# Kernel tuning notes

Hardware: AMD Instinct MI355X
Metric: run time of the kernel (lower is better)

## Reference

```python
import jax, jax.numpy as jnp
import numpy as np

B, S, D, A = 64, 2048, 512, 512


def setup_inputs() -> dict:
    key = jax.random.key(0)
    ks = jax.random.split(key, 6)
    return {
        "input": jax.random.normal(ks[0], (B, D), dtype=jnp.float32),
        "context": jax.random.normal(ks[1], (B, S, D), dtype=jnp.float32),
        "Wh": jax.random.uniform(ks[2], (D, A), dtype=jnp.float32, minval=-0.1, maxval=0.1),
        "Ws": jax.random.uniform(ks[3], (D, A), dtype=jnp.float32, minval=-0.1, maxval=0.1),
        "b_attn": jax.random.uniform(ks[4], (A,), dtype=jnp.float32, minval=-0.1, maxval=0.1),
        "va": jax.random.uniform(ks[5], (A,), dtype=jnp.float32, minval=-0.1, maxval=0.1),
    }


def reference(input, context, Wh, Ws, b_attn, va):
    # _concat score: tanh(ht@Wh + context@Ws + b) @ va  -> [B, S]
    ht_proj = input @ Wh                      # [B, A]
    ctx_proj = jnp.einsum("bsd,da->bsa", context, Ws)  # [B, S, A]
    concat = jnp.tanh(ht_proj[:, None, :] + ctx_proj + b_attn)  # [B, S, A]
    attn = jnp.einsum("bsa,a->bs", concat, va)  # [B, S]
    # padding mask: positions whose mean feature is exactly 0
    context_mask = jnp.mean(context, axis=-1) == 0  # [B, S]
    attn = jnp.where(context_mask, -jnp.inf, attn)
    attn_dist = jax.nn.softmax(attn, axis=1)  # [B, S]
    attn_context = jnp.einsum("bsd,bs->bd", context, attn_dist)  # [B, D]
    return attn_context, attn_dist
```

## Files before the change

kernel.cpp:

```cpp
#include <hip/hip_runtime.h>
#include <hip/hip_bf16.h>
#include <math.h>

#define B_ 64
#define S_ 2048
#define D_ 512
#define A_ 512

typedef __attribute__((ext_vector_type(8))) short short8;
typedef __attribute__((ext_vector_type(4))) short short4b;
typedef __attribute__((ext_vector_type(4))) float f32x4;

__device__ __forceinline__ short bf16b(float f) {
    __hip_bfloat16 h = __float2bfloat16(f);
    union { __hip_bfloat16 h; short s; } u; u.h = h;
    return u.s;
}

__device__ __forceinline__ float tanh_fast(float x) {
    float e = __expf(2.0f * x);
    return 1.0f - 2.0f / (e + 1.0f);
}

__device__ __forceinline__ void llds16(const void* g, void* l) {
    __builtin_amdgcn_global_load_lds(
        (const __attribute__((address_space(1))) unsigned int*)g,
        (__attribute__((address_space(3))) unsigned int*)l, 16, 0, 0);
}

__global__ __launch_bounds__(256) void k_htw(const float* __restrict__ input,
                                             const float* __restrict__ Wh,
                                             const float* __restrict__ b_attn,
                                             float* __restrict__ htWb) {
    __shared__ float xin[512];
    const int b = blockIdx.x, t = threadIdx.x;
    xin[t] = input[b * D_ + t];
    xin[t + 256] = input[b * D_ + t + 256];
    __syncthreads();
    float a0 = 0.f, a1 = 0.f;
#pragma unroll 8
    for (int d = 0; d < D_; ++d) {
        const float xv = xin[d];
        a0 += xv * Wh[d * A_ + t];
        a1 += xv * Wh[d * A_ + t + 256];
    }
    htWb[b * A_ + t] = a0 + b_attn[t];
    htWb[b * A_ + t + 256] = a1 + b_attn[t + 256];
}

__global__ __launch_bounds__(256) void k_wst(const float* __restrict__ Ws,
                                             short* __restrict__ WsT) {
    const int bx = blockIdx.x & 7, by = blockIdx.x >> 3;
    const int r0 = by * 64, c0 = bx * 64;
    __shared__ short tile[64][72];
    const int t = threadIdx.x;
    const int row = t >> 4, col4 = (t & 15) * 4;
#pragma unroll
    for (int i = 0; i < 4; ++i) {
        const float4 v = *(const float4*)&Ws[(r0 + row + i * 16) * A_ + c0 + col4];
        tile[col4 + 0][row + i * 16] = bf16b(v.x);
        tile[col4 + 1][row + i * 16] = bf16b(v.y);
        tile[col4 + 2][row + i * 16] = bf16b(v.z);
        tile[col4 + 3][row + i * 16] = bf16b(v.w);
    }
    __syncthreads();
#pragma unroll
    for (int i = 0; i < 4; ++i) {
        const int arow = row + i * 16;
        short4b o;
        o.x = tile[arow][col4 + 0];
        o.y = tile[arow][col4 + 1];
        o.z = tile[arow][col4 + 2];
        o.w = tile[arow][col4 + 3];
        *(short4b*)&WsT[(c0 + arow) * D_ + r0 + col4] = o;
    }
}

__global__ __launch_bounds__(512, 2)
void k_score2(const float* __restrict__ ctx, const short* __restrict__ WsT,
              const float* __restrict__ htWb, const float* __restrict__ va,
              float* __restrict__ scores) {
    __shared__ __align__(16) short Ab[2][128 * 32];
    __shared__ __align__(16) short Bb[2][512 * 32];
    __shared__ float hv_s[512];
    __shared__ float va_s[512];
    __shared__ float scores_s[128];
    __shared__ float rowsum_s[128];

    const int tid = threadIdx.x;
    const int w = tid >> 6, lane = tid & 63;
    const int wm = w >> 2, wn = w & 3;
    const int blk = blockIdx.x;
    const int b = blk >> 4;
    const int s0 = (blk & 15) * 128;
    const long rowbase = (long)b * S_ + s0;

    hv_s[tid] = htWb[b * A_ + tid];
    va_s[tid] = va[tid];
    if (tid < 128) scores_s[tid] = 0.f;

    const int arow = tid >> 2, aq = tid & 2 * 2 - 1;
    const float* aSrc = ctx + (rowbase + arow) * (long)D_;
    float rowsum_acc = 0.f;

    f32x4 acc[4][8];
#pragma unroll
    for (int i = 0; i < 4; ++i)
#pragma unroll
        for (int j = 0; j < 8; ++j)
#pragma unroll
            for (int e = 0; e < 4; ++e) acc[i][j][e] = 0.f;

#define STAGE_B(buf, kt)                                                      \
    {                                                                         \
        _Pragma("unroll") for (int j = 0; j < 4; ++j) {                       \
            const int a = (w * 4 + j) * 16 + (lane >> 2);                     \
            const int c = lane & 3;                                           \
            const int csw = c ^ ((a >> 1) & 3);                               \
            llds16(WsT + a * D_ + (kt) * 32 + csw * 8,                        \
                   (void*)&Bb[buf][(w * 4 + j) * 512]);                       \
        }                                                                     \
    }

#define STAGE_A_WRITE(buf, v0, v1)                                            \
    {                                                                         \
        rowsum_acc += (v0).x + (v0).y + (v0).z + (v0).w;                      \
        rowsum_acc += (v1).x + (v1).y + (v1).z + (v1).w;                      \
        short4b o0, o1;                                                       \
        o0.x = bf16b((v0).x); o0.y = bf16b((v0).y);                           \
        o0.z = bf16b((v0).z); o0.w = bf16b((v0).w);                           \
        o1.x = bf16b((v1).x); o1.y = bf16b((v1).y);                           \
        o1.z = bf16b((v1).z); o1.w = bf16b((v1).w);                           \
        const int sw = (arow >> 1) & 3;                                       \
        const int c0 = (aq >> 1), c1 = 2 + (aq >> 1), sub = aq & 1;           \
        *(short4b*)((char*)&Ab[buf][0] + arow * 64 + ((c0 ^ sw) * 16) + sub * 8) = o0; \
        *(short4b*)((char*)&Ab[buf][0] + arow * 64 + ((c1 ^ sw) * 16) + sub * 8) = o1; \
    }

    STAGE_B(0, 0);
    {
        const float4 v0 = *(const float4*)(aSrc + aq * 4);
        const float4 v1 = *(const float4*)(aSrc + aq * 4 + 16);
        STAGE_A_WRITE(0, v0, v1);
    }
    __syncthreads();

    for (int kt = 0; kt < 16; ++kt) {
        const int cur = kt & 1;
        float4 nv0, nv1;
        if (kt < 15) {
            STAGE_B(cur ^ 1, kt + 1);
            nv0 = *(const float4*)(aSrc + (kt + 1) * 32 + aq * 4);
            nv1 = *(const float4*)(aSrc + (kt + 1) * 32 + aq * 4 + 16);
        }
        {
            short8 af[4];
#pragma unroll
            for (int mf = 0; mf < 4; ++mf) {
                const int r = wm * 64 + mf * 16 + (lane & 15);
                const int c = lane >> 4;
                const int csw = c ^ ((r >> 1) & 3);
                af[mf] = *(const short8*)((const char*)&Ab[cur][0] + r * 64 + csw * 16);
            }
#pragma unroll
            for (int nf = 0; nf < 8; ++nf) {
                const int a = wn * 128 + nf * 16 + (lane & 15);
                const int c = lane >> 4;
                const int csw = c ^ ((a >> 1) & 3);
                const short8 bf =
                    *(const short8*)((const char*)&Bb[cur][0] + a * 64 + csw * 16);
#pragma unroll
                for (int mf = 0; mf < 4; ++mf)
                    acc[mf][nf] = __builtin_amdgcn_mfma_f32_16x16x32_bf16(
                        af[mf], bf, acc[mf][nf], 0, 0, 0);
            }
        }
        if (kt < 15) STAGE_A_WRITE(cur ^ 1, nv0, nv1);
        __syncthreads();
    }

    rowsum_acc += __shfl_xor(rowsum_acc, 1);
    rowsum_acc += __shfl_xor(rowsum_acc, 2);
    if ((tid & 3) == 0) rowsum_s[arow] = rowsum_acc;

    float hv[8], vv[8];
#pragma unroll
    for (int nf = 0; nf < 8; ++nf) {
        const int col = wn * 128 + nf * 16 + (lane & 15);
        hv[nf] = hv_s[col];
        vv[nf] = va_s[col];
    }
#pragma unroll
    for (int mf = 0; mf < 4; ++mf) {
#pragma unroll
        for (int e = 0; e < 4; ++e) {
            float p = 0.f;
#pragma unroll
            for (int nf = 0; nf < 8; ++nf)
                p += vv[nf] * tanh_fast(hv[nf] + acc[mf][nf][e]);
            p += __shfl_xor(p, 1);
            p += __shfl_xor(p, 2);
            p += __shfl_xor(p, 4);
            p += __shfl_xor(p, 8);
            if ((lane & 15) == 0) {
                const int row = wm * 64 + mf * 16 + (lane >> 4) * 4 + e;
                atomicAdd(&scores_s[row], p);
            }
        }
    }
    __syncthreads();

    if (tid < 128) {
        float sc = scores_s[tid];
        if (rowsum_s[tid] == 0.0f) sc = -__builtin_inff();
        scores[rowbase + tid] = sc;
    }
}

__global__ __launch_bounds__(256) void k_softmax(float* __restrict__ dist) {
    const int b = blockIdx.x, t = threadIdx.x;
    float* p = dist + b * S_;
    float v[8];
    float m = -__builtin_inff();
#pragma unroll
    for (int i = 0; i < 8; ++i) {
        v[i] = p[t + i * 256];
        m = fmaxf(m, v[i]);
    }
#pragma unroll
    for (int mask = 1; mask < 64; mask <<= 1) m = fmaxf(m, __shfl_xor(m, mask));
    __shared__ float redm[4], reds[4];
    if ((t & 63) == 0) redm[t >> 6] = m;
    __syncthreads();
    m = fmaxf(fmaxf(redm[0], redm[1]), fmaxf(redm[2], redm[3]));
    float sum = 0.f;
#pragma unroll
    for (int i = 0; i < 8; ++i) {
        v[i] = __expf(v[i] - m);
        sum += v[i];
    }
#pragma unroll
    for (int mask = 1; mask < 64; mask <<= 1) sum += __shfl_xor(sum, mask);
    if ((t & 63) == 0) reds[t >> 6] = sum;
    __syncthreads();
    sum = reds[0] + reds[1] + reds[2] + reds[3];
    const float inv = 1.0f / sum;
#pragma unroll
    for (int i = 0; i < 8; ++i) p[t + i * 256] = v[i] * inv;
}

__global__ __launch_bounds__(128) void k_wsum(const float* __restrict__ ctx,
                                              const float* __restrict__ dist,
                                              float* __restrict__ partial) {
    const int ch = blockIdx.x, b = blockIdx.y;
    const int t = threadIdx.x;
    __shared__ float ps[128];
    ps[t] = dist[b * S_ + ch * 128 + t];
    __syncthreads();
    const float* cbase = ctx + ((long)b * S_ + ch * 128) * D_;
    float ax = 0.f, ay = 0.f, az = 0.f, aw = 0.f;
#pragma unroll 4
    for (int r = 0; r < 128; ++r) {
        const float4 cv = *(const float4*)&cbase[r * D_ + t * 4];
        const float pw = ps[r];
        ax += pw * cv.x;
        ay += pw * cv.y;
        az += pw * cv.z;
        aw += pw * cv.w;
    }
    float4 o; o.x = ax; o.y = ay; o.z = az; o.w = aw;
    *(float4*)&partial[((b * 16 + ch) * D_) + t * 4] = o;
}

__global__ __launch_bounds__(128) void k_reduce(const float* __restrict__ partial,
                                                float* __restrict__ out) {
    const int b = blockIdx.x, t = threadIdx.x;
    float ax = 0.f, ay = 0.f, az = 0.f, aw = 0.f;
#pragma unroll
    for (int j = 0; j < 16; ++j) {
        const float4 v = *(const float4*)&partial[((b * 16 + j) * D_) + t * 4];
        ax += v.x; ay += v.y; az += v.z; aw += v.w;
    }
    float4 o; o.x = ax; o.y = ay; o.z = az; o.w = aw;
    *(float4*)&out[b * D_ + t * 4] = o;
}

extern "C" void kernel_launch(void* const* d_in, const int* in_sizes, int n_in,
                              void* d_out, int out_size, void* d_ws, size_t ws_size,
                              hipStream_t stream) {
    (void)in_sizes; (void)n_in; (void)out_size; (void)ws_size;
    const float* input  = (const float*)d_in[0];
    const float* ctx    = (const float*)d_in[1];
    const float* Wh     = (const float*)d_in[2];
    const float* Ws     = (const float*)d_in[3];
    const float* b_attn = (const float*)d_in[4];
    const float* va     = (const float*)d_in[5];

    float* out = (float*)d_out;
    float* attn_ctx  = out;
    float* attn_dist = out + B_ * D_;

    char* ws = (char*)d_ws;
    float* htWb    = (float*)ws;
    short* WsT     = (short*)(ws + 131072);
    float* partial = (float*)(ws + 131072 + 524288);

    k_htw<<<64, 256, 0, stream>>>(input, Wh, b_attn, htWb);
    k_wst<<<64, 256, 0, stream>>>(Ws, WsT);
    k_score2<<<1024, 512, 0, stream>>>(ctx, WsT, htWb, va, attn_dist);
    k_softmax<<<64, 256, 0, stream>>>(attn_dist);
    k_wsum<<<dim3(16, 64), 128, 0, stream>>>(ctx, attn_dist, partial);
    k_reduce<<<64, 128, 0, stream>>>(partial, attn_ctx);
}
```

Baseline: 519.5 us.

## Merge prep kernels, single-buffer A tile with manual waits, split wsum rows

Fuses the htW projection and Ws transpose kernels into one launch to save a kernel launch. The score kernel switches the A tile to a single LDS buffer, issues context loads through inline asm with explicit vmcnt/lgkmcnt waits, sched barriers and raised wave priority around the MFMA block. This frees LDS and is meant to let global loads overlap compute, at the cost of an extra barrier per iteration. k_wsum doubles threads per block, splits rows into two halves and reduces through LDS to add memory-level parallelism.

```diff
diff --git a/kernel.cpp b/kernel.cpp
--- a/kernel.cpp
+++ b/kernel.cpp
@@ -28,60 +28,62 @@
         (__attribute__((address_space(3))) unsigned int*)l, 16, 0, 0);
 }
 
-__global__ __launch_bounds__(256) void k_htw(const float* __restrict__ input,
-                                             const float* __restrict__ Wh,
-                                             const float* __restrict__ b_attn,
-                                             float* __restrict__ htWb) {
-    __shared__ float xin[512];
-    const int b = blockIdx.x, t = threadIdx.x;
-    xin[t] = input[b * D_ + t];
-    xin[t + 256] = input[b * D_ + t + 256];
-    __syncthreads();
-    float a0 = 0.f, a1 = 0.f;
+__global__ __launch_bounds__(256) void k_prep(const float* __restrict__ input,
+                                              const float* __restrict__ Wh,
+                                              const float* __restrict__ b_attn,
+                                              const float* __restrict__ Ws,
+                                              float* __restrict__ htWb,
+                                              short* __restrict__ WsT) {
+    const int t = threadIdx.x;
+    if (blockIdx.x < 64) {
+        __shared__ float xin[512];
+        const int b = blockIdx.x;
+        xin[t] = input[b * D_ + t];
+        xin[t + 256] = input[b * D_ + t + 256];
+        __syncthreads();
+        float a0 = 0.f, a1 = 0.f;
 #pragma unroll 8
-    for (int d = 0; d < D_; ++d) {
-        const float xv = xin[d];
-        a0 += xv * Wh[d * A_ + t];
-        a1 += xv * Wh[d * A_ + t + 256];
-    }
-    htWb[b * A_ + t] = a0 + b_attn[t];
-    htWb[b * A_ + t + 256] = a1 + b_attn[t + 256];
-}
-
-__global__ __launch_bounds__(256) void k_wst(const float* __restrict__ Ws,
-                                             short* __restrict__ WsT) {
-    const int bx = blockIdx.x & 7, by = blockIdx.x >> 3;
-    const int r0 = by * 64, c0 = bx * 64;
-    __shared__ short tile[64][72];
-    const int t = threadIdx.x;
-    const int row = t >> 4, col4 = (t & 15) * 4;
-#pragma unroll
-    for (int i = 0; i < 4; ++i) {
-        const float4 v = *(const float4*)&Ws[(r0 + row + i * 16) * A_ + c0 + col4];
-        tile[col4 + 0][row + i * 16] = bf16b(v.x);
-        tile[col4 + 1][row + i * 16] = bf16b(v.y);
-        tile[col4 + 2][row + i * 16] = bf16b(v.z);
-        tile[col4 + 3][row + i * 16] = bf16b(v.w);
-    }
-    __syncthreads();
-#pragma unroll
-    for (int i = 0; i < 4; ++i) {
-        const int arow = row + i * 16;
-        short4b o;
-        o.x = tile[arow][col4 + 0];
-        o.y = tile[arow][col4 + 1];
-        o.z = tile[arow][col4 + 2];
-        o.w = tile[arow][col4 + 3];
-        *(short4b*)&WsT[(c0 + arow) * D_ + r0 + col4] = o;
+        for (int d = 0; d < D_; ++d) {
+            const float xv = xin[d];
+            a0 += xv * Wh[d * A_ + t];
+            a1 += xv * Wh[d * A_ + t + 256];
+        }
+        htWb[b * A_ + t] = a0 + b_attn[t];
+        htWb[b * A_ + t + 256] = a1 + b_attn[t + 256];
+    } else {
+        const int blk = blockIdx.x - 64;
+        const int bx = blk & 7, by = blk >> 3;
+        const int r0 = by * 64, c0 = bx * 64;
+        __shared__ short tile[64][72];
+        const int row = t >> 4, col4 = (t & 15) * 4;
+#pragma unroll
+        for (int i = 0; i < 4; ++i) {
+            const float4 v = *(const float4*)&Ws[(r0 + row + i * 16) * A_ + c0 + col4];
+            tile[col4 + 0][row + i * 16] = bf16b(v.x);
+            tile[col4 + 1][row + i * 16] = bf16b(v.y);
+            tile[col4 + 2][row + i * 16] = bf16b(v.z);
+            tile[col4 + 3][row + i * 16] = bf16b(v.w);
+        }
+        __syncthreads();
+#pragma unroll
+        for (int i = 0; i < 4; ++i) {
+            const int arow = row + i * 16;
+            short4b o;
+            o.x = tile[arow][col4 + 0];
+            o.y = tile[arow][col4 + 1];
+            o.z = tile[arow][col4 + 2];
+            o.w = tile[arow][col4 + 3];
+            *(short4b*)&WsT[(c0 + arow) * D_ + r0 + col4] = o;
+        }
     }
 }
 
 __global__ __launch_bounds__(512, 2)
-void k_score2(const float* __restrict__ ctx, const short* __restrict__ WsT,
+void k_score3(const float* __restrict__ ctx, const short* __restrict__ WsT,
               const float* __restrict__ htWb, const float* __restrict__ va,
               float* __restrict__ scores) {
-    __shared__ __align__(16) short Ab[2][128 * 32];
     __shared__ __align__(16) short Bb[2][512 * 32];
+    __shared__ __align__(16) short Ab[128 * 32];
     __shared__ float hv_s[512];
     __shared__ float va_s[512];
     __shared__ float scores_s[128];
@@ -99,7 +101,7 @@
     va_s[tid] = va[tid];
     if (tid < 128) scores_s[tid] = 0.f;
 
-    const int arow = tid >> 2, aq = tid & 2 * 2 - 1;
+    const int arow = tid >> 2, aq = tid & 3;
     const float* aSrc = ctx + (rowbase + arow) * (long)D_;
     float rowsum_acc = 0.f;
 
@@ -122,37 +124,41 @@
         }                                                                     \
     }
 
-#define STAGE_A_WRITE(buf, v0, v1)                                            \
+#define STAGE_A_WRITE(v0, v1)                                                 \
     {                                                                         \
-        rowsum_acc += (v0).x + (v0).y + (v0).z + (v0).w;                      \
-        rowsum_acc += (v1).x + (v1).y + (v1).z + (v1).w;                      \
+        rowsum_acc += (v0)[0] + (v0)[1] + (v0)[2] + (v0)[3];                  \
+        rowsum_acc += (v1)[0] + (v1)[1] + (v1)[2] + (v1)[3];                  \
         short4b o0, o1;                                                       \
-        o0.x = bf16b((v0).x); o0.y = bf16b((v0).y);                           \
-        o0.z = bf16b((v0).z); o0.w = bf16b((v0).w);                           \
-        o1.x = bf16b((v1).x); o1.y = bf16b((v1).y);                           \
-        o1.z = bf16b((v1).z); o1.w = bf16b((v1).w);                           \
+        o0.x = bf16b((v0)[0]); o0.y = bf16b((v0)[1]);                         \
+        o0.z = bf16b((v0)[2]); o0.w = bf16b((v0)[3]);                         \
+        o1.x = bf16b((v1)[0]); o1.y = bf16b((v1)[1]);                         \
+        o1.z = bf16b((v1)[2]); o1.w = bf16b((v1)[3]);                         \
         const int sw = (arow >> 1) & 3;                                       \
-        const int c0 = (aq >> 1), c1 = 2 + (aq >> 1), sub = aq & 1;           \
-        *(short4b*)((char*)&Ab[buf][0] + arow * 64 + ((c0 ^ sw) * 16) + sub * 8) = o0; \
-        *(short4b*)((char*)&Ab[buf][0] + arow * 64 + ((c1 ^ sw) * 16) + sub * 8) = o1; \
-    }
-
-    STAGE_B(0, 0);
+        const int c0g = (aq >> 1), c1g = 2 + (aq >> 1), sub = aq & 1;         \
+        *(short4b*)((char*)Ab + arow * 64 + ((c0g ^ sw) * 16) + sub * 8) = o0; \
+        *(short4b*)((char*)Ab + arow * 64 + ((c1g ^ sw) * 16) + sub * 8) = o1; \
+    }
+
     {
-        const float4 v0 = *(const float4*)(aSrc + aq * 4);
-        const float4 v1 = *(const float4*)(aSrc + aq * 4 + 16);
-        STAGE_A_WRITE(0, v0, v1);
+        const f32x4 v0 = *(const f32x4*)(aSrc + aq * 4);
+        const f32x4 v1 = *(const f32x4*)(aSrc + aq * 4 + 16);
+        STAGE_B(0, 0);
+        STAGE_A_WRITE(v0, v1);
     }
     __syncthreads();
 
     for (int kt = 0; kt < 16; ++kt) {
         const int cur = kt & 1;
-        float4 nv0, nv1;
+        f32x4 nv0, nv1;
         if (kt < 15) {
+            const float* p0 = aSrc + (kt + 1) * 32 + aq * 4;
+            asm volatile("global_load_dwordx4 %0, %1, off" : "=v"(nv0) : "v"(p0));
+            asm volatile("global_load_dwordx4 %0, %1, off" : "=v"(nv1) : "v"(p0 + 16));
+            __builtin_amdgcn_sched_barrier(0);
             STAGE_B(cur ^ 1, kt + 1);
-            nv0 = *(const float4*)(aSrc + (kt + 1) * 32 + aq * 4);
-            nv1 = *(const float4*)(aSrc + (kt + 1) * 32 + aq * 4 + 16);
-        }
+            __builtin_amdgcn_sched_barrier(0);
+        }
+        __builtin_amdgcn_s_setprio(1);
         {
             short8 af[4];
 #pragma unroll
@@ -160,7 +166,7 @@
                 const int r = wm * 64 + mf * 16 + (lane & 15);
                 const int c = lane >> 4;
                 const int csw = c ^ ((r >> 1) & 3);
-                af[mf] = *(const short8*)((const char*)&Ab[cur][0] + r * 64 + csw * 16);
+                af[mf] = *(const short8*)((const char*)Ab + r * 64 + csw * 16);
             }
 #pragma unroll
             for (int nf = 0; nf < 8; ++nf) {
@@ -175,7 +181,15 @@
                         af[mf], bf, acc[mf][nf], 0, 0, 0);
             }
         }
-        if (kt < 15) STAGE_A_WRITE(cur ^ 1, nv0, nv1);
+        __builtin_amdgcn_s_setprio(0);
+        asm volatile("s_waitcnt lgkmcnt(0)" ::: "memory");
+        __builtin_amdgcn_sched_barrier(0);
+        __builtin_amdgcn_s_barrier();
+        if (kt < 15) {
+            asm volatile("s_waitcnt vmcnt(4)" ::: "memory");
+            __builtin_amdgcn_sched_barrier(0);
+            STAGE_A_WRITE(nv0, nv1);
+        }
         __syncthreads();
     }
 
@@ -249,27 +263,35 @@
     for (int i = 0; i < 8; ++i) p[t + i * 256] = v[i] * inv;
 }
 
-__global__ __launch_bounds__(128) void k_wsum(const float* __restrict__ ctx,
+__global__ __launch_bounds__(256) void k_wsum(const float* __restrict__ ctx,
                                               const float* __restrict__ dist,
                                               float* __restrict__ partial) {
     const int ch = blockIdx.x, b = blockIdx.y;
     const int t = threadIdx.x;
+    const int half = t >> 7;
+    const int td = (t & 127) * 4;
     __shared__ float ps[128];
-    ps[t] = dist[b * S_ + ch * 128 + t];
-    __syncthreads();
-    const float* cbase = ctx + ((long)b * S_ + ch * 128) * D_;
-    float ax = 0.f, ay = 0.f, az = 0.f, aw = 0.f;
+    __shared__ f32x4 red[128];
+    if (t < 128) ps[t] = dist[b * S_ + ch * 128 + t];
+    __syncthreads();
+    const float* cbase = ctx + ((long)b * S_ + ch * 128 + half * 64) * D_ + td;
+    f32x4 a = {0.f, 0.f, 0.f, 0.f};
 #pragma unroll 4
-    for (int r = 0; r < 128; ++r) {
-        const float4 cv = *(const float4*)&cbase[r * D_ + t * 4];
-        const float pw = ps[r];
-        ax += pw * cv.x;
-        ay += pw * cv.y;
-        az += pw * cv.z;
-        aw += pw * cv.w;
-    }
-    float4 o; o.x = ax; o.y = ay; o.z = az; o.w = aw;
-    *(float4*)&partial[((b * 16 + ch) * D_) + t * 4] = o;
+    for (int r = 0; r < 64; ++r) {
+        const f32x4 cv = *(const f32x4*)(cbase + (long)r * D_);
+        const float pw = ps[half * 64 + r];
+        a[0] += pw * cv[0];
+        a[1] += pw * cv[1];
+        a[2] += pw * cv[2];
+        a[3] += pw * cv[3];
+    }
+    if (half == 1) red[t & 127] = a;
+    __syncthreads();
+    if (half == 0) {
+        const f32x4 o = red[t];
+        a[0] += o[0]; a[1] += o[1]; a[2] += o[2]; a[3] += o[3];
+        *(f32x4*)&partial[((b * 16 + ch) * D_) + td] = a;
+    }
 }
 
 __global__ __launch_bounds__(128) void k_reduce(const float* __restrict__ partial,
@@ -305,10 +327,9 @@
     short* WsT     = (short*)(ws + 131072);
     float* partial = (float*)(ws + 131072 + 524288);
 
-    k_htw<<<64, 256, 0, stream>>>(input, Wh, b_attn, htWb);
-    k_wst<<<64, 256, 0, stream>>>(Ws, WsT);
-    k_score2<<<1024, 512, 0, stream>>>(ctx, WsT, htWb, va, attn_dist);
+    k_prep<<<128, 256, 0, stream>>>(input, Wh, b_attn, Ws, htWb, WsT);
+    k_score3<<<1024, 512, 0, stream>>>(ctx, WsT, htWb, va, attn_dist);
     k_softmax<<<64, 256, 0, stream>>>(attn_dist);
-    k_wsum<<<dim3(16, 64), 128, 0, stream>>>(ctx, attn_dist, partial);
+    k_wsum<<<dim3(16, 64), 256, 0, stream>>>(ctx, attn_dist, partial);
     k_reduce<<<64, 128, 0, stream>>>(partial, attn_ctx);
 }
```

Measured after the change: 516.2 us. Within noise of the previous version (-0.6%).
